# Performance work log

Measured on AMD Instinct MI355X. Metric: run time of the kernel, lower is better.

Reference implementation:

```python
import jax, jax.numpy as jnp
import numpy as np

B, S, D, H = 4, 1024, 1024, 16
HD = D // H
MAX_DIST, WIN, MAX_SPAN = 512, 256, 512
TEMP_SCALE = 0.01
EPS = 1e-5


def _ln(x, g, b):
    m = x.mean(-1, keepdims=True)
    v = ((x - m) ** 2).mean(-1, keepdims=True)
    return (x - m) * jax.lax.rsqrt(v + EPS) * g + b


def _heads(t):
    b, s, _ = t.shape
    return t.reshape(b, s, H, HD).transpose(0, 2, 1, 3)


def _merge(t):
    b, _, s, _ = t.shape
    return t.transpose(0, 2, 1, 3).reshape(b, s, D)


def _global_attn(x, Wq, bq, Wk, Wv, bv, Wo, bo):
    # MultiheadC with mask tensor passed -> is_causal=True SDPA (default 1/sqrt(HD) scale)
    q = _heads(x @ Wq.T + bq)
    k = _heads(x @ Wk.T)
    v = _heads(x @ Wv.T + bv)
    s = jnp.einsum('bhqd,bhkd->bhqk', q, k) / float(np.sqrt(HD))
    n = x.shape[1]
    causal = jnp.tril(jnp.ones((n, n), bool))
    s = jnp.where(causal, s, jnp.finfo(s.dtype).min)
    w = jax.nn.softmax(s, axis=-1)
    return _merge(jnp.einsum('bhqk,bhkd->bhqd', w, v)) @ Wo.T + bo


def _span_attn(q, k, v, temp):
    # AdaptiveSpan core: softmax(QK^T / temperature * head_dim**-0.25) V
    scale = HD ** -0.25
    qh, kh, vh = _heads(q), _heads(k), _heads(v)
    w = jax.nn.softmax(jnp.einsum('bhqd,bhkd->bhqk', qh, kh) / temp * scale, axis=-1)
    return _merge(jnp.einsum('bhqk,bhkd->bhqd', w, vh))


def _slide_win(local, span_mean, win, span_len, local_max):
    bx, sx, dx = local.shape
    temp = 1.0 + TEMP_SCALE * (1.0 - span_mean)  # sharpen=True branch
    outs = []
    for st in range(0, sx, win):  # static unrolled loop over windows (ragged slices)
        en = min(st + win, sx)
        wlen = en - st
        ks = max(0, st - span_len + win)
        ke = min(st + span_len, sx)
        klen = ke - ks
        eff = min(int(wlen * span_mean), wlen, klen, local_max)
        if eff <= 0:
            outs.append(jnp.zeros((bx, wlen, dx), local.dtype))
            continue
        o = _span_attn(local[:, st:st + eff], local[:, ks:ks + eff], local[:, ks:ks + eff], temp)
        if eff < wlen:
            o = jnp.concatenate([o, jnp.zeros((bx, wlen - eff, dx), local.dtype)], axis=1)
        outs.append(o)
    return jnp.concatenate(outs, axis=1)


def setup_inputs() -> dict:
    key = jax.random.key(0)
    ks = jax.random.split(key, 8)
    qkv_std = 1.0 / float(np.sqrt(HD))
    return {
        'x': jax.random.normal(ks[0], (B, S, D), jnp.float32),
        'ln_a_g': jnp.ones((D,), jnp.float32),
        'ln_a_b': jnp.zeros((D,), jnp.float32),
        'ln_b_g': jnp.ones((D,), jnp.float32),
        'ln_b_b': jnp.zeros((D,), jnp.float32),
        'Wq': jax.random.normal(ks[1], (D, D), jnp.float32) * qkv_std,
        'bq': jnp.zeros((D,), jnp.float32),
        'Wk': jax.random.normal(ks[2], (D, D), jnp.float32) * qkv_std,
        'Wv': jax.random.normal(ks[3], (D, D), jnp.float32) * qkv_std,
        'bv': jnp.zeros((D,), jnp.float32),
        'Wo': jax.random.normal(ks[4], (D, D), jnp.float32) * 0.02,
        'bo': jnp.zeros((D,), jnp.float32),
        'Wp': jax.random.normal(ks[5], (1, D), jnp.float32) * float(np.sqrt(2.0 / (D + 1))),
        'bp': jnp.zeros((1,), jnp.float32),
        'Wproj': jax.random.normal(ks[6], (D, 2 * D), jnp.float32) * 0.02,
        'bproj': jnp.zeros((D,), jnp.float32),
    }


def reference(x, ln_a_g, ln_a_b, ln_b_g, ln_b_b, Wq, bq, Wk, Wv, bv, Wo, bo, Wp, bp, Wproj, bproj):
    local = _ln(x, ln_a_g, ln_a_b)
    globe = _ln(x, ln_b_g, ln_b_b)
    globe_out = _global_attn(globe, Wq, bq, Wk, Wv, bv, Wo, bo)
    # Predictor: sigmoid(Linear(mean over seq))
    base_scale = jax.nn.sigmoid(globe_out.mean(axis=1) @ Wp.T + bp)  # [B, 1]
    span_scale = jnp.clip(base_scale, 0.0, 1.0)  # RL refine factor fixed at 1.0 (deterministic)
    span_mean = float(jnp.mean(span_scale))  # mirrors torch .item() host sync
    win = max(1, int(WIN * span_mean))
    span_len = max(1, int(MAX_SPAN * span_mean))
    local_max = min(MAX_DIST, span_len, win)
    local_out = _slide_win(local, span_mean, win, span_len, local_max)
    combined = jnp.concatenate([local_out, globe_out], axis=-1)
    return combined @ Wproj.T + bproj
```

## Files before the change

kernel.cpp:

```cpp
#include <hip/hip_runtime.h>
#include <math.h>

#define B_ 4
#define S_ 1024
#define D_ 1024
#define H_ 16
#define HD_ 64
#define BSD_ (B_*S_*D_)

using short8 = __attribute__((ext_vector_type(8))) short;
using f32x4  = __attribute__((ext_vector_type(4))) float;

#define MFMA16(a,b,c) __builtin_amdgcn_mfma_f32_16x16x32_bf16((a),(b),(c),0,0,0)

__device__ __forceinline__ ushort f2bf(float f) {
  uint u = __float_as_uint(f);
  return (ushort)((u + 0x7fffu + ((u >> 16) & 1u)) >> 16);
}
__device__ __forceinline__ float bf2f(ushort h) {
  return __uint_as_float(((uint)h) << 16);
}
__device__ __forceinline__ void split8(const float* p, short8* hi, short8* lo) {
  #pragma unroll
  for (int j = 0; j < 8; j++) {
    ushort h = f2bf(p[j]);
    (*hi)[j] = (short)h;
    (*lo)[j] = (short)f2bf(p[j] - bf2f(h));
  }
}
__device__ __forceinline__ void async_load16(const ushort* g, ushort* l) {
  __builtin_amdgcn_global_load_lds(
      (const __attribute__((address_space(1))) unsigned int*)g,
      (__attribute__((address_space(3))) unsigned int*)l, 16, 0, 0);
}

__device__ __forceinline__ float block_reduce_sum_256(float v, float* sbuf) {
  #pragma unroll
  for (int off = 32; off > 0; off >>= 1) v += __shfl_xor(v, off, 64);
  int lane = threadIdx.x & 63, wid = threadIdx.x >> 6;
  __syncthreads();
  if (lane == 0) sbuf[wid] = v;
  __syncthreads();
  return sbuf[0] + sbuf[1] + sbuf[2] + sbuf[3];
}

__device__ __forceinline__ void split4_store(const float4 a, ushort* orow, int c, int stride) {
  ushort4 hi, lo;
  hi.x = f2bf(a.x); hi.y = f2bf(a.y); hi.z = f2bf(a.z); hi.w = f2bf(a.w);
  lo.x = f2bf(a.x - bf2f(hi.x)); lo.y = f2bf(a.y - bf2f(hi.y));
  lo.z = f2bf(a.z - bf2f(hi.z)); lo.w = f2bf(a.w - bf2f(hi.w));
  *(ushort4*)(orow + c)          = hi;
  *(ushort4*)(orow + stride + c) = lo;
}

__global__ __launch_bounds__(256) void prep_kernel(
    const float* __restrict__ x,
    const float* __restrict__ ln_a_g, const float* __restrict__ ln_a_b,
    const float* __restrict__ ln_b_g, const float* __restrict__ ln_b_b,
    const float* __restrict__ Wq, const float* __restrict__ Wk,
    const float* __restrict__ Wv, const float* __restrict__ bq,
    const float* __restrict__ bv, const float* __restrict__ Wo,
    const float* __restrict__ Wproj,
    ushort* __restrict__ Acat, ushort* __restrict__ Bqkv,
    float* __restrict__ biascat, float* __restrict__ loc,
    ushort* __restrict__ B3, ushort* __restrict__ Bo) {
  __shared__ float sbuf[4];
  const int bx = blockIdx.x;
  const int t = threadIdx.x;
  if (bx < 4096) {
    const int row = bx;
    const int c = t*4;
    const float* xr = x + (size_t)row * D_;
    float4 v = *(const float4*)(xr + c);
    float s = v.x + v.y + v.z + v.w;
    const float mean = block_reduce_sum_256(s, sbuf) * (1.0f/D_);
    float4 dv = make_float4(v.x-mean, v.y-mean, v.z-mean, v.w-mean);
    float sq = dv.x*dv.x + dv.y*dv.y + dv.z*dv.z + dv.w*dv.w;
    const float var = block_reduce_sum_256(sq, sbuf) * (1.0f/D_);
    const float r = rsqrtf(var + 1e-5f);
    float4 gg = *(const float4*)(ln_b_g + c);
    float4 bb = *(const float4*)(ln_b_b + c);
    float4 n;
    n.x = dv.x*r*gg.x + bb.x; n.y = dv.y*r*gg.y + bb.y;
    n.z = dv.z*r*gg.z + bb.z; n.w = dv.w*r*gg.w + bb.w;
    split4_store(n, Acat + (size_t)row*2048, c, 1024);
  } else if (bx < 7168) {
    const int idx = (bx - 4096)*256 + t;
    const int n = idx >> 8;
    const int col4 = (idx & 255) << 2;
    const float* src = (n < 1024) ? (Wq + (size_t)n*1024)
                     : (n < 2048) ? (Wk + (size_t)(n-1024)*1024)
                                  : (Wv + (size_t)(n-2048)*1024);
    const float4 a = *(const float4*)(src + col4);
    split4_store(a, Bqkv + (size_t)n*2048, col4, 1024);
    if (idx < 3072)
      biascat[idx] = (idx < 1024) ? bq[idx] : (idx < 2048) ? 0.f : bv[idx-2048];
  } else if (bx < 11264) {
    const int row = bx - 7168;
    const float* xr = x + (size_t)row * D_;
    float v[4]; float s = 0.f;
    #pragma unroll
    for (int i = 0; i < 4; i++) { v[i] = xr[t + 256*i]; s += v[i]; }
    const float mean = block_reduce_sum_256(s, sbuf) * (1.0f/D_);
    float sq = 0.f;
    #pragma unroll
    for (int i = 0; i < 4; i++) { float d = v[i]-mean; sq += d*d; }
    const float var = block_reduce_sum_256(sq, sbuf) * (1.0f/D_);
    const float r = rsqrtf(var + 1e-5f);
    float* orow = loc + (size_t)row * D_;
    #pragma unroll
    for (int i = 0; i < 4; i++) {
      int c = t + 256*i;
      orow[c] = (v[i]-mean)*r*ln_a_g[c] + ln_a_b[c];
    }
  } else if (bx < 13312) {
    const int idx = (bx - 11264)*256 + t;
    const int row = idx >> 9;
    const int col4 = (idx & 511) << 2;
    const float4 a = *(const float4*)(Wproj + (size_t)row*2048 + col4);
    ushort4 hi;
    hi.x = f2bf(a.x); hi.y = f2bf(a.y); hi.z = f2bf(a.z); hi.w = f2bf(a.w);
    *(ushort4*)(B3 + (size_t)row*2048 + col4) = hi;
  } else {
    const int idx = (bx - 13312)*256 + t;
    const int n = idx >> 8;
    const int col4 = (idx & 255) << 2;
    const float4 a = *(const float4*)(Wo + (size_t)n*1024 + col4);
    split4_store(a, Bo + (size_t)n*2048, col4, 1024);
  }
}

#define BARRIER() asm volatile("s_barrier" ::: "memory")
#define VMW(n)  asm volatile("s_waitcnt vmcnt(" #n ")" ::: "memory")

#define STAGE4(k0, SBs) do { \
  _Pragma("unroll") \
  for (int i_ = 0; i_ < 2; ++i_) { \
    const int cid_ = wave*2 + i_, hl_ = cid_>>2, rs_ = cid_&3; \
    const int r0_ = (rs_>>1)*64 + (rs_&1)*16; \
    async_load16(A  + ((size_t)(bm + r0_ + lrow) << 11) + (hl_ << 10) + (k0) + sw, \
                 (SBs) + hl_*4096 + r0_*32); \
  } \
  _Pragma("unroll") \
  for (int i_ = 0; i_ < 2; ++i_) { \
    const int cid_ = wave*2 + i_, hl_ = cid_>>2, rs_ = cid_&3; \
    const int r0_ = (rs_>>1)*64 + (rs_&1)*16; \
    async_load16(Bw + ((size_t)(bn + r0_ + lrow) << 11) + (hl_ << 10) + (k0) + sw, \
                 (SBs) + 8192 + hl_*4096 + r0_*32); \
  } \
  _Pragma("unroll") \
  for (int i_ = 0; i_ < 2; ++i_) { \
    const int cid_ = wave*2 + i_, hl_ = cid_>>2, rs_ = cid_&3; \
    const int r1_ = (rs_>>1)*64 + (rs_&1)*16 + 32; \
    async_load16(Bw + ((size_t)(bn + r1_ + lrow) << 11) + (hl_ << 10) + (k0) + sw, \
                 (SBs) + 8192 + hl_*4096 + r1_*32); \
  } \
  _Pragma("unroll") \
  for (int i_ = 0; i_ < 2; ++i_) { \
    const int cid_ = wave*2 + i_, hl_ = cid_>>2, rs_ = cid_&3; \
    const int r1_ = (rs_>>1)*64 + (rs_&1)*16 + 32; \
    async_load16(A  + ((size_t)(bm + r1_ + lrow) << 11) + (hl_ << 10) + (k0) + sw, \
                 (SBs) + hl_*4096 + r1_*32); \
  } \
} while (0)

#define PH4(mh, nh, SBc, STG, WT) do { \
  short8 ah_[2], al_[2], bh_[2], bl_[2]; \
  _Pragma("unroll") \
  for (int m4_ = 0; m4_ < 2; ++m4_) { \
    const int ro_ = (wm*64 + (mh)*32 + m4_*16 + lm)*32 + rsw; \
    ah_[m4_] = *(const short8*)&(SBc)[ro_]; \
    al_[m4_] = *(const short8*)&(SBc)[4096 + ro_]; } \
  _Pragma("unroll") \
  for (int n2_ = 0; n2_ < 2; ++n2_) { \
    const int ro_ = (wn*64 + (nh)*32 + n2_*16 + lm)*32 + rsw; \
    bh_[n2_] = *(const short8*)&(SBc)[8192 + ro_]; \
    bl_[n2_] = *(const short8*)&(SBc)[12288 + ro_]; } \
  STG; \
  WT; \
  BARRIER(); \
  __builtin_amdgcn_s_setprio(1); \
  _Pragma("unroll") \
  for (int m4_ = 0; m4_ < 2; ++m4_) \
    _Pragma("unroll") \
    for (int n2_ = 0; n2_ < 2; ++n2_) { \
      f32x4 t_ = acc[(mh)*2+m4_][(nh)*2+n2_]; \
      t_ = MFMA16(ah_[m4_], bh_[n2_], t_); \
      t_ = MFMA16(al_[m4_], bh_[n2_], t_); \
      t_ = MFMA16(ah_[m4_], bl_[n2_], t_); \
      acc[(mh)*2+m4_][(nh)*2+n2_] = t_; } \
  __builtin_amdgcn_s_setprio(0); \
  BARRIER(); \
} while (0)

#define GROUP4(g, SBc, SBs) do { \
  const int k0n_ = (((g) + 1) & 31) * 32; \
  PH4(0, 0, (SBc), STAGE4(k0n_, (SBs)), VMW(10)); \
  PH4(0, 1, (SBc), ((void)0), VMW(8)); \
  PH4(1, 0, (SBc), ((void)0), ((void)0)); \
  PH4(1, 1, (SBc), ((void)0), VMW(4)); \
} while (0)

__global__ __launch_bounds__(256, 2) void qkv4_kernel(
    const ushort* __restrict__ A, const ushort* __restrict__ Bw,
    const float* __restrict__ bias,
    ushort* __restrict__ Qsp, ushort* __restrict__ Ksp,
    ushort* __restrict__ Vth, ushort* __restrict__ Vtl) {
  extern __shared__ __align__(16) ushort smem[];
  const int tid = threadIdx.x;
  const int bm = blockIdx.y * 128, bn = blockIdx.x * 128;
  const int wave = tid >> 6, lane = tid & 63;
  const int wm = wave >> 1, wn = wave & 1;
  const int lm = lane & 15, q = lane >> 4;
  const int lrow = lane >> 2;
  const int sw = (((lane & 3) ^ ((lane >> 3) & 3)) << 3);
  const int rsw = ((q ^ ((lm >> 1) & 3)) << 3);

  f32x4 acc[4][4];
  #pragma unroll
  for (int i = 0; i < 4; i++)
    #pragma unroll
    for (int j = 0; j < 4; j++)
      acc[i][j] = (f32x4){0.f,0.f,0.f,0.f};

  STAGE4(0, smem);
  VMW(4); BARRIER();

  #pragma unroll 1
  for (int g = 0; g < 32; g += 2) {
    GROUP4(g,     smem,         smem + 16384);
    GROUP4(g + 1, smem + 16384, smem);
  }
  VMW(0);
  __syncthreads();

  const int b = bm >> 10, s0 = bm & 1023;
  if (blockIdx.x < 16) {
    ushort* dst = (blockIdx.x < 8) ? Qsp : Ksp;
    #pragma unroll
    for (int mt = 0; mt < 4; mt++) {
      #pragma unroll
      for (int nt = 0; nt < 4; nt++) {
        const int n = bn + wn*64 + nt*16 + lm;
        const int h = (n >> 6) & 15;
        const int d = nt*16 + lm;
        const float bb = bias[n];
        #pragma unroll
        for (int reg = 0; reg < 4; reg++) {
          const int s = s0 + wm*64 + mt*16 + q*4 + reg;
          const float val = acc[mt][nt][reg] + bb;
          const ushort hi = f2bf(val);
          const ushort lo = f2bf(val - bf2f(hi));
          ushort* rp = dst + ((size_t)((b*16 + h)*1024 + s))*128;
          rp[d] = hi; rp[64 + d] = lo;
        }
      }
    }
  } else {
    ushort* Th = smem;
    ushort* Tl = smem + 8704;
    #pragma unroll
    for (int c = 0; c < 2; c++) {
      __syncthreads();
      if (wn == c) {
        #pragma unroll
        for (int mt = 0; mt < 4; mt++)
          #pragma unroll
          for (int nt = 0; nt < 4; nt++) {
            const int nl = nt*16 + lm;
            const float bb = bias[bn + c*64 + nl];
            #pragma unroll
            for (int reg = 0; reg < 4; reg++) {
              const int sl = wm*64 + mt*16 + q*4 + reg;
              const float val = acc[mt][nt][reg] + bb;
              const ushort hi = f2bf(val);
              const ushort lo = f2bf(val - bf2f(hi));
              Th[nl*136 + sl] = hi;
              Tl[nl*136 + sl] = lo;
            }
          }
      }
      __syncthreads();
      const int nl = tid >> 2, s32 = (tid & 3)*32;
      const int h = ((bn - 2048 + c*64) >> 6) & 15;
      const size_t drow = ((size_t)((b*16 + h)*64 + nl))*1024 + s0 + s32;
      #pragma unroll
      for (int j = 0; j < 4; j++) {
        *(short8*)(Vth + drow + j*8) = *(const short8*)&Th[nl*136 + s32 + j*8];
        *(short8*)(Vtl + drow + j*8) = *(const short8*)&Tl[nl*136 + s32 + j*8];
      }
    }
  }
}

__global__ __launch_bounds__(256) void mfma_gemm_qkv(
    const ushort* __restrict__ A, const ushort* __restrict__ Bw,
    const float* __restrict__ bias,
    ushort* __restrict__ Qsp, ushort* __restrict__ Ksp,
    ushort* __restrict__ Vth, ushort* __restrict__ Vtl, int Kh) {
  __shared__ __align__(16) ushort smem[17408];
  ushort* Ash = smem;
  ushort* Asl = smem + 4096;
  ushort* Bsh = smem + 8192;
  ushort* Bsl = smem + 12288;
  const int lda = 2*Kh;
  const int tid = threadIdx.x;
  const int bm = blockIdx.y * 128, bn = blockIdx.x * 128;
  const int wave = tid >> 6, lane = tid & 63;
  const int wm = wave >> 1, wn = wave & 1;
  const int lm = lane & 15, q = lane >> 4;
  const int lrow = lane >> 2;
  const int sw = (((lane & 3) ^ ((lane >> 3) & 3)) << 3);

  f32x4 acc[4][4];
  #pragma unroll
  for (int i = 0; i < 4; i++)
    #pragma unroll
    for (int j = 0; j < 4; j++)
      acc[i][j] = (f32x4){0.f,0.f,0.f,0.f};

  const ushort* Agh = A  + (size_t)(bm + wave*32 + lrow)*lda + sw;
  const ushort* Agl = Agh + Kh;
  const ushort* Bgh = Bw + (size_t)(bn + wave*32 + lrow)*lda + sw;
  const ushort* Bgl = Bgh + Kh;
  const size_t r16a = (size_t)16*lda;
  ushort* AhD0 = &Ash[(wave*32)*32];      ushort* AhD1 = &Ash[(wave*32+16)*32];
  ushort* AlD0 = &Asl[(wave*32)*32];      ushort* AlD1 = &Asl[(wave*32+16)*32];
  ushort* BhD0 = &Bsh[(wave*32)*32];      ushort* BhD1 = &Bsh[(wave*32+16)*32];
  ushort* BlD0 = &Bsl[(wave*32)*32];      ushort* BlD1 = &Bsl[(wave*32+16)*32];
  const int rsw  = ((q ^ ((lm >> 1) & 3)) << 3);
  const int aoff = (wm*64 + lm)*32 + rsw;
  const int boff = (wn*64 + lm)*32 + rsw;

  for (int k0 = 0; k0 < Kh; k0 += 32) {
    __syncthreads();
    async_load16(Agh + k0, AhD0);
    async_load16(Agh + r16a + k0, AhD1);
    async_load16(Agl + k0, AlD0);
    async_load16(Agl + r16a + k0, AlD1);
    async_load16(Bgh + k0, BhD0);
    async_load16(Bgh + r16a + k0, BhD1);
    async_load16(Bgl + k0, BlD0);
    async_load16(Bgl + r16a + k0, BlD1);
    __syncthreads();
    short8 ah[4], al[4], bh[4], bl[4];
    #pragma unroll
    for (int mt = 0; mt < 4; mt++) {
      ah[mt] = *(const short8*)&Ash[aoff + mt*512];
      al[mt] = *(const short8*)&Asl[aoff + mt*512];
    }
    #pragma unroll
    for (int nt = 0; nt < 4; nt++) {
      bh[nt] = *(const short8*)&Bsh[boff + nt*512];
      bl[nt] = *(const short8*)&Bsl[boff + nt*512];
    }
    #pragma unroll
    for (int mt = 0; mt < 4; mt++)
      #pragma unroll
      for (int nt = 0; nt < 4; nt++) {
        f32x4 a = acc[mt][nt];
        a = MFMA16(ah[mt], bh[nt], a);
        a = MFMA16(al[mt], bh[nt], a);
        a = MFMA16(ah[mt], bl[nt], a);
        acc[mt][nt] = a;
      }
  }

  const int b = bm >> 10, s0 = bm & 1023;
  if (blockIdx.x < 16) {
    ushort* dst = (blockIdx.x < 8) ? Qsp : Ksp;
    #pragma unroll
    for (int mt = 0; mt < 4; mt++) {
      #pragma unroll
      for (int nt = 0; nt < 4; nt++) {
        const int n = bn + wn*64 + nt*16 + lm;
        const int h = (n >> 6) & 15;
        const int d = nt*16 + lm;
        const float bb = bias[n];
        #pragma unroll
        for (int reg = 0; reg < 4; reg++) {
          const int s = s0 + wm*64 + mt*16 + q*4 + reg;
          const float val = acc[mt][nt][reg] + bb;
          const ushort hi = f2bf(val);
          const ushort lo = f2bf(val - bf2f(hi));
          ushort* rp = dst + ((size_t)((b*16 + h)*1024 + s))*128;
          rp[d] = hi; rp[64 + d] = lo;
        }
      }
    }
  } else {
    ushort* Th = smem;
    ushort* Tl = smem + 8704;
    #pragma unroll
    for (int c = 0; c < 2; c++) {
      __syncthreads();
      if (wn == c) {
        #pragma unroll
        for (int mt = 0; mt < 4; mt++)
          #pragma unroll
          for (int nt = 0; nt < 4; nt++) {
            const int nl = nt*16 + lm;
            const float bb = bias[bn + c*64 + nl];
            #pragma unroll
            for (int reg = 0; reg < 4; reg++) {
              const int sl = wm*64 + mt*16 + q*4 + reg;
              const float val = acc[mt][nt][reg] + bb;
              const ushort hi = f2bf(val);
              const ushort lo = f2bf(val - bf2f(hi));
              Th[nl*136 + sl] = hi;
              Tl[nl*136 + sl] = lo;
            }
          }
      }
      __syncthreads();
      const int nl = tid >> 2, s32 = (tid & 3)*32;
      const int h = ((bn - 2048 + c*64) >> 6) & 15;
      const size_t drow = ((size_t)((b*16 + h)*64 + nl))*1024 + s0 + s32;
      #pragma unroll
      for (int j = 0; j < 4; j++) {
        *(short8*)(Vth + drow + j*8) = *(const short8*)&Th[nl*136 + s32 + j*8];
        *(short8*)(Vtl + drow + j*8) = *(const short8*)&Tl[nl*136 + s32 + j*8];
      }
    }
  }
}

__global__ __launch_bounds__(256) void mfma_gemm2(
    const ushort* __restrict__ A, const ushort* __restrict__ Bw,
    const float* __restrict__ bias, float* __restrict__ C,
    int Kh, int ldc, ushort* __restrict__ aux) {
  __shared__ __align__(16) ushort Ash[64*32];
  __shared__ __align__(16) ushort Asl[64*32];
  __shared__ __align__(16) ushort Bsh[128*32];
  __shared__ __align__(16) ushort Bsl[128*32];
  const int lda = 2*Kh;
  const int tid = threadIdx.x;
  const int bm = blockIdx.y * 64, bn = blockIdx.x * 128;
  const int wave = tid >> 6, lane = tid & 63;
  const int lm = lane & 15, q = lane >> 4;
  const int lrow = lane >> 2;
  const int sw = (((lane & 3) ^ ((lane >> 3) & 3)) << 3);

  f32x4 acc[4][2];
  #pragma unroll
  for (int i = 0; i < 4; i++)
    #pragma unroll
    for (int j = 0; j < 2; j++)
      acc[i][j] = (f32x4){0.f,0.f,0.f,0.f};

  const ushort* gsrc[6];
  ushort* ldst[6];
  #pragma unroll
  for (int i = 0; i < 6; i++) {
    const int s = wave*6 + i;
    const ushort* gp; ushort* lp;
    if (s < 4)       { gp = A  + (size_t)(bm + s*16 + lrow)*lda + sw;           lp = &Ash[(s*16)*32]; }
    else if (s < 8)  { gp = A  + (size_t)(bm + (s-4)*16 + lrow)*lda + Kh + sw;  lp = &Asl[((s-4)*16)*32]; }
    else if (s < 16) { gp = Bw + (size_t)(bn + (s-8)*16 + lrow)*lda + sw;       lp = &Bsh[((s-8)*16)*32]; }
    else             { gp = Bw + (size_t)(bn + (s-16)*16 + lrow)*lda + Kh + sw; lp = &Bsl[((s-16)*16)*32]; }
    gsrc[i] = gp; ldst[i] = lp;
  }
  const int rsw = ((q ^ ((lm >> 1) & 3)) << 3);
  const int aoff = lm*32 + rsw;
  const int boff = (wave*32 + lm)*32 + rsw;

  for (int k0 = 0; k0 < Kh; k0 += 32) {
    __syncthreads();
    #pragma unroll
    for (int i = 0; i < 6; i++) async_load16(gsrc[i] + k0, ldst[i]);
    __syncthreads();
    short8 ah[4], al[4], bh[2], bl[2];
    #pragma unroll
    for (int mt = 0; mt < 4; mt++) {
      ah[mt] = *(const short8*)&Ash[aoff + mt*512];
      al[mt] = *(const short8*)&Asl[aoff + mt*512];
    }
    #pragma unroll
    for (int nt = 0; nt < 2; nt++) {
      bh[nt] = *(const short8*)&Bsh[boff + nt*512];
      bl[nt] = *(const short8*)&Bsl[boff + nt*512];
    }
    #pragma unroll
    for (int mt = 0; mt < 4; mt++)
      #pragma unroll
      for (int nt = 0; nt < 2; nt++) {
        f32x4 a = acc[mt][nt];
        a = MFMA16(ah[mt], bh[nt], a);
        a = MFMA16(al[mt], bh[nt], a);
        a = MFMA16(ah[mt], bl[nt], a);
        acc[mt][nt] = a;
      }
  }

  #pragma unroll
  for (int mt = 0; mt < 4; mt++) {
    #pragma unroll
    for (int nt = 0; nt < 2; nt++) {
      const int n = bn + wave*32 + nt*16 + lm;
      const float bb = bias ? bias[n] : 0.f;
      #pragma unroll
      for (int reg = 0; reg < 4; reg++) {
        const int m = bm + mt*16 + q*4 + reg;
        const float val = acc[mt][nt][reg] + bb;
        C[(size_t)m*ldc + n] = val;
        if (aux) aux[(size_t)m*2048 + 1024 + n] = f2bf(val);
      }
    }
  }
}

__global__ __launch_bounds__(256) void mfma_gemm(
    const ushort* __restrict__ A, const ushort* __restrict__ Bw,
    const float* __restrict__ bias, float* __restrict__ C,
    int K, int ldc) {
  __shared__ __align__(16) ushort As[64*32];
  __shared__ __align__(16) ushort Bs[128*32];
  const int tid = threadIdx.x;
  const int bm = blockIdx.y * 64, bn = blockIdx.x * 128;
  const int wave = tid >> 6, lane = tid & 63;
  const int lm = lane & 15, q = lane >> 4;
  const int lrow = lane >> 2;
  const int sw = (((lane & 3) ^ ((lane >> 3) & 3)) << 3);

  f32x4 acc[4][2];
  #pragma unroll
  for (int i = 0; i < 4; i++)
    #pragma unroll
    for (int j = 0; j < 2; j++)
      acc[i][j] = (f32x4){0.f,0.f,0.f,0.f};

  const ushort* gsrc[3];
  ushort* ldst[3];
  #pragma unroll
  for (int i = 0; i < 3; i++) {
    const int s = wave*3 + i;
    const ushort* gp; ushort* lp;
    if (s < 4) { gp = A  + (size_t)(bm + s*16 + lrow)*K + sw;     lp = &As[(s*16)*32]; }
    else       { gp = Bw + (size_t)(bn + (s-4)*16 + lrow)*K + sw; lp = &Bs[((s-4)*16)*32]; }
    gsrc[i] = gp; ldst[i] = lp;
  }
  const int rsw = ((q ^ ((lm >> 1) & 3)) << 3);
  const int aoff = lm*32 + rsw;
  const int boff = (wave*32 + lm)*32 + rsw;

  for (int k0 = 0; k0 < K; k0 += 32) {
    __syncthreads();
    #pragma unroll
    for (int i = 0; i < 3; i++) async_load16(gsrc[i] + k0, ldst[i]);
    __syncthreads();
    short8 af[4], bf[2];
    #pragma unroll
    for (int mt = 0; mt < 4; mt++) af[mt] = *(const short8*)&As[aoff + mt*512];
    #pragma unroll
    for (int nt = 0; nt < 2; nt++) bf[nt] = *(const short8*)&Bs[boff + nt*512];
    #pragma unroll
    for (int mt = 0; mt < 4; mt++)
      #pragma unroll
      for (int nt = 0; nt < 2; nt++)
        acc[mt][nt] = MFMA16(af[mt], bf[nt], acc[mt][nt]);
  }

  #pragma unroll
  for (int mt = 0; mt < 4; mt++) {
    #pragma unroll
    for (int nt = 0; nt < 2; nt++) {
      const int n = bn + wave*32 + nt*16 + lm;
      const float bb = bias ? bias[n] : 0.f;
      #pragma unroll
      for (int reg = 0; reg < 4; reg++) {
        const int m = bm + mt*16 + q*4 + reg;
        C[(size_t)m*ldc + n] = acc[mt][nt][reg] + bb;
      }
    }
  }
}

__device__ __forceinline__ void attn_unit(
    int qt, int kt, int w, int lm, int q,
    const short8 qh[2], const short8 ql[2],
    const ushort* Kc, const ushort* Vc, float* Pf,
    f32x4 of[4], float mst[4], float lst[4]) {
  f32x4 sS[4];
  #pragma unroll
  for (int nt = 0; nt < 4; nt++) {
    const ushort* kr = &Kc[(nt*16 + lm)*136 + q*8];
    const short8 kh0 = *(const short8*)(kr);
    const short8 kh1 = *(const short8*)(kr + 32);
    const short8 kl0 = *(const short8*)(kr + 64);
    const short8 kl1 = *(const short8*)(kr + 96);
    f32x4 a = (f32x4){0.f,0.f,0.f,0.f};
    a = MFMA16(qh[0], kh0, a);
    a = MFMA16(ql[0], kh0, a);
    a = MFMA16(qh[0], kl0, a);
    a = MFMA16(qh[1], kh1, a);
    a = MFMA16(ql[1], kh1, a);
    a = MFMA16(qh[1], kl1, a);
    sS[nt] = a;
  }
  const int ktbase = kt*64;
  const int qrow0 = qt*64 + w*16 + q*4;
  #pragma unroll
  for (int rm = 0; rm < 4; rm++) {
    const int qrow = qrow0 + rm;
    float v[4];
    #pragma unroll
    for (int nt = 0; nt < 4; nt++) {
      const int kcol = ktbase + nt*16 + lm;
      const float x = sS[nt][rm]*0.125f;
      v[nt] = (kcol <= qrow) ? x : -INFINITY;
    }
    float tm = fmaxf(fmaxf(v[0],v[1]), fmaxf(v[2],v[3]));
    #pragma unroll
    for (int off = 1; off < 16; off <<= 1) tm = fmaxf(tm, __shfl_xor(tm, off, 64));
    const float nm = fmaxf(mst[rm], tm);
    const float alpha = __expf(mst[rm] - nm);
    float ps = 0.f;
    #pragma unroll
    for (int nt = 0; nt < 4; nt++) {
      float p = __expf(v[nt] - nm);
      sS[nt][rm] = p;
      ps += p;
    }
    #pragma unroll
    for (int off = 1; off < 16; off <<= 1) ps += __shfl_xor(ps, off, 64);
    lst[rm] = lst[rm]*alpha + ps;
    mst[rm] = nm;
    #pragma unroll
    for (int nt = 0; nt < 4; nt++) of[nt][rm] *= alpha;
  }
  #pragma unroll
  for (int rm = 0; rm < 4; rm++)
    #pragma unroll
    for (int nt = 0; nt < 4; nt++)
      Pf[(w*16 + q*4 + rm)*66 + nt*16 + lm] = sS[nt][rm];
  short8 ph[2], pl[2];
  {
    const float* prow = &Pf[(w*16 + lm)*66];
    float pv[16];
    *(float4*)&pv[0]  = *(const float4*)(prow + q*8);
    *(float4*)&pv[4]  = *(const float4*)(prow + q*8 + 4);
    *(float4*)&pv[8]  = *(const float4*)(prow + 32 + q*8);
    *(float4*)&pv[12] = *(const float4*)(prow + 32 + q*8 + 4);
    split8(&pv[0], &ph[0], &pl[0]);
    split8(&pv[8], &ph[1], &pl[1]);
  }
  #pragma unroll
  for (int nt = 0; nt < 4; nt++) {
    const ushort* vr = &Vc[(nt*16 + lm)*136 + q*8];
    const short8 vh0 = *(const short8*)(vr);
    const short8 vh1 = *(const short8*)(vr + 32);
    const short8 vl0 = *(const short8*)(vr + 64);
    const short8 vl1 = *(const short8*)(vr + 96);
    f32x4 a = of[nt];
    a = MFMA16(ph[0], vh0, a);
    a = MFMA16(pl[0], vh0, a);
    a = MFMA16(ph[0], vl0, a);
    a = MFMA16(ph[1], vh1, a);
    a = MFMA16(pl[1], vh1, a);
    a = MFMA16(ph[1], vl1, a);
    of[nt] = a;
  }
}

__global__ __launch_bounds__(256) void gattn_mfma(
    const ushort* __restrict__ Qsp, const ushort* __restrict__ Ksp,
    const ushort* __restrict__ Vth, const ushort* __restrict__ Vtl,
    ushort* __restrict__ Aout) {
  __shared__ __align__(16) ushort Kc[64*136];
  __shared__ __align__(16) ushort Vc[64*136];
  __shared__ __align__(16) float  Pf[64*66];
  const int bh = blockIdx.y;
  const int b = bh >> 4, h = bh & 15;
  const int tid = threadIdx.x;
  const int w = tid >> 6, lane = tid & 63;
  const int lm = lane & 15, q = lane >> 4;
  const ushort* Qb_ = Qsp + (size_t)bh * (1024*128);
  const ushort* Kb_ = Ksp + (size_t)bh * (1024*128);
  const ushort* Vhb = Vth + (size_t)bh * (64*1024);
  const ushort* Vlb = Vtl + (size_t)bh * (64*1024);
  const int qtA = 15 - blockIdx.x;
  const int qtB = blockIdx.x;

  short8 qhA[2], qlA[2], qhB[2], qlB[2];
  {
    const ushort* qr = Qb_ + (size_t)(qtA*64 + w*16 + lm)*128 + q*8;
    qhA[0] = *(const short8*)(qr);
    qhA[1] = *(const short8*)(qr + 32);
    qlA[0] = *(const short8*)(qr + 64);
    qlA[1] = *(const short8*)(qr + 96);
    const ushort* qr2 = Qb_ + (size_t)(qtB*64 + w*16 + lm)*128 + q*8;
    qhB[0] = *(const short8*)(qr2);
    qhB[1] = *(const short8*)(qr2 + 32);
    qlB[0] = *(const short8*)(qr2 + 64);
    qlB[1] = *(const short8*)(qr2 + 96);
  }
  f32x4 ofA[4], ofB[4];
  float mstA[4], lstA[4], mstB[4], lstB[4];
  #pragma unroll
  for (int nt = 0; nt < 4; nt++) {
    ofA[nt] = (f32x4){0.f,0.f,0.f,0.f};
    ofB[nt] = (f32x4){0.f,0.f,0.f,0.f};
  }
  #pragma unroll
  for (int rm = 0; rm < 4; rm++) {
    mstA[rm] = -INFINITY; lstA[rm] = 0.f;
    mstB[rm] = -INFINITY; lstB[rm] = 0.f;
  }

  for (int kt = 0; kt <= qtA; ++kt) {
    __syncthreads();
    #pragma unroll
    for (int i = 0; i < 4; i++) {
      const int slot = i*256 + tid;
      const int row = slot >> 4, c8 = slot & 15;
      *(float4*)&Kc[row*136 + c8*8] =
          *(const float4*)(Kb_ + (size_t)(kt*64 + row)*128 + c8*8);
      const ushort* vsrc = ((c8 < 8) ? Vhb : Vlb) + (size_t)row*1024 + kt*64 + (c8&7)*8;
      *(float4*)&Vc[row*136 + c8*8] = *(const float4*)vsrc;
    }
    __syncthreads();
    attn_unit(qtA, kt, w, lm, q, qhA, qlA, Kc, Vc, Pf, ofA, mstA, lstA);
    if (kt <= qtB)
      attn_unit(qtB, kt, w, lm, q, qhB, qlB, Kc, Vc, Pf, ofB, mstB, lstB);
  }

  #pragma unroll
  for (int rm = 0; rm < 4; rm++) {
    const float invA = 1.0f / lstA[rm];
    const int sA = qtA*64 + w*16 + q*4 + rm;
    ushort* arow = Aout + ((size_t)(b*1024 + sA))*2048 + h*64;
    #pragma unroll
    for (int nt = 0; nt < 4; nt++) {
      const float val = ofA[nt][rm] * invA;
      const ushort hi = f2bf(val);
      arow[nt*16 + lm] = hi;
      arow[1024 + nt*16 + lm] = f2bf(val - bf2f(hi));
    }
    const float invB = 1.0f / lstB[rm];
    const int sB = qtB*64 + w*16 + q*4 + rm;
    ushort* brow = Aout + ((size_t)(b*1024 + sB))*2048 + h*64;
    #pragma unroll
    for (int nt = 0; nt < 4; nt++) {
      const float val = ofB[nt][rm] * invB;
      const ushort hi = f2bf(val);
      brow[nt*16 + lm] = hi;
      brow[1024 + nt*16 + lm] = f2bf(val - bf2f(hi));
    }
  }
}

__global__ __launch_bounds__(256) void seqmean1_kernel(const float* __restrict__ g,
                                                       float* __restrict__ part) {
  const int d = blockIdx.x*256 + threadIdx.x;
  const int sc = blockIdx.y;
  const int b = blockIdx.z;
  const float* p = g + ((size_t)b*S_ + sc*128)*D_ + d;
  float s = 0.f;
  #pragma unroll 4
  for (int i = 0; i < 128; i++) s += p[(size_t)i*D_];
  part[((size_t)(b*8 + sc))*D_ + d] = s;
}
__global__ __launch_bounds__(256) void seqmean2_kernel(const float* __restrict__ part,
                                                       float* __restrict__ mbd) {
  const int d = blockIdx.x*256 + threadIdx.x;
  const int b = blockIdx.y;
  float s = 0.f;
  #pragma unroll
  for (int i = 0; i < 8; i++) s += part[((size_t)(b*8 + i))*D_ + d];
  mbd[b*D_ + d] = s * (1.0f/S_);
}

__global__ __launch_bounds__(256) void predictor_kernel(
    const float* __restrict__ mbd, const float* __restrict__ Wp,
    const float* __restrict__ bp, float* __restrict__ fpar, int* __restrict__ ipar) {
  __shared__ float sbuf[4];
  __shared__ float sdots[4];
  const int tid = threadIdx.x;
  for (int b = 0; b < 4; b++) {
    float psum = 0.f;
    for (int d = tid; d < D_; d += 256) psum += mbd[b*D_ + d]*Wp[d];
    float tot = block_reduce_sum_256(psum, sbuf);
    if (tid == 0) sdots[b] = tot;
  }
  __syncthreads();
  if (tid == 0) {
    float smv = 0.f;
    for (int b = 0; b < 4; b++) {
      float z = sdots[b] + bp[0];
      smv += 1.0f/(1.0f + expf(-z));
    }
    smv *= 0.25f;
    int win = max(1, (int)(256.0f*smv));
    int span_len = max(1, (int)(512.0f*smv));
    int local_max = min(512, min(span_len, win));
    float temp = 1.0f + 0.01f*(1.0f - smv);
    int n_win = (S_ + win - 1)/win;
    fpar[0] = smv; fpar[1] = temp;
    ipar[0] = win; ipar[1] = span_len; ipar[2] = local_max; ipar[3] = n_win;
  }
}

#define LDP 68
__global__ __launch_bounds__(256) void lattn_kernel(
    const float* __restrict__ Lc, ushort* __restrict__ Out,
    const int* __restrict__ ip, const float* __restrict__ fpp) {
  __shared__ __align__(16) float Qs[HD_][LDP];
  __shared__ __align__(16) float KPs[64][LDP];
  __shared__ __align__(16) float Vs[64][LDP];
  const int n_win = ip[3];
  const int win = ip[0], span_len = ip[1], local_max = ip[2];
  const float sm = fpp[0], temp = fpp[1];
  const int bh = blockIdx.y;
  const int b = bh >> 4, h = bh & 15;
  const int tid = threadIdx.x;
  const int tx = tid & 15, ty = tid >> 4;
  const float sc = 0.35355339059327373f / temp;
  for (int w = blockIdx.x; w < n_win; w += gridDim.x) {
    const int st = w * win;
    const int en = min(st + win, S_); const int wlen = en - st;
    const int ks = max(0, st - span_len + win);
    const int ke = min(st + span_len, S_); const int klen = ke - ks;
    int eff = (int)((double)wlen * (double)sm);
    eff = min(min(eff, wlen), min(klen, local_max));
    if (eff > 0) {
      const int nt = (eff + 63) >> 6;
      for (int qt = 0; qt < nt; ++qt) {
        const int qn = min(64, eff - qt*64);
        __syncthreads();
        #pragma unroll
        for (int c = 0; c < 4; c++) {
          int f = tid + c*256;
          int r = f >> 4;
          int dc = (f & 15) << 2;
          float4 q4 = make_float4(0.f,0.f,0.f,0.f);
          if (r < qn) q4 = *(const float4*)(Lc + ((size_t)(b*S_ + st + qt*64 + r)) * D_ + h*HD_ + dc);
          Qs[dc+0][r]=q4.x; Qs[dc+1][r]=q4.y; Qs[dc+2][r]=q4.z; Qs[dc+3][r]=q4.w;
        }
        float o[4][4] = {{0.f,0.f,0.f,0.f},{0.f,0.f,0.f,0.f},{0.f,0.f,0.f,0.f},{0.f,0.f,0.f,0.f}};
        float mrow[4], lrow[4];
        #pragma unroll
        for (int i=0;i<4;i++){ mrow[i] = -INFINITY; lrow[i] = 0.f; }
        for (int kt = 0; kt < nt; ++kt) {
          const int kn = min(64, eff - kt*64);
          __syncthreads();
          #pragma unroll
          for (int c = 0; c < 4; c++) {
            int f = tid + c*256;
            int r = f >> 4;
            int dc = (f & 15) << 2;
            float4 k4 = make_float4(0.f,0.f,0.f,0.f);
            if (r < kn) k4 = *(const float4*)(Lc + ((size_t)(b*S_ + ks + kt*64 + r)) * D_ + h*HD_ + dc);
            KPs[dc+0][r]=k4.x; KPs[dc+1][r]=k4.y; KPs[dc+2][r]=k4.z; KPs[dc+3][r]=k4.w;
            *(float4*)&Vs[r][dc] = k4;
          }
          __syncthreads();
          float s[4][4] = {{0.f,0.f,0.f,0.f},{0.f,0.f,0.f,0.f},{0.f,0.f,0.f,0.f},{0.f,0.f,0.f,0.f}};
          #pragma unroll 8
          for (int d = 0; d < HD_; ++d) {
            const float4 a  = *(const float4*)&Qs[d][ty*4];
            const float4 bb = *(const float4*)&KPs[d][tx*4];
            const float av[4]={a.x,a.y,a.z,a.w};
            const float bv[4]={bb.x,bb.y,bb.z,bb.w};
            #pragma unroll
            for (int i=0;i<4;i++)
              #pragma unroll
              for (int j=0;j<4;j++)
                s[i][j] += av[i]*bv[j];
          }
          #pragma unroll
          for (int i=0;i<4;i++) {
            #pragma unroll
            for (int j=0;j<4;j++) {
              float lg = s[i][j]*sc;
              if (kt*64 + tx*4 + j >= eff) lg = -INFINITY;
              s[i][j] = lg;
            }
          }
          #pragma unroll
          for (int i=0;i<4;i++) {
            float tm = fmaxf(fmaxf(s[i][0],s[i][1]), fmaxf(s[i][2],s[i][3]));
            #pragma unroll
            for (int off=1; off<16; off<<=1) tm = fmaxf(tm, __shfl_xor(tm, off, 64));
            const float nm = fmaxf(mrow[i], tm);
            const float alpha = __expf(mrow[i]-nm);
            float ps = 0.f;
            #pragma unroll
            for (int j=0;j<4;j++){ float p = __expf(s[i][j]-nm); s[i][j]=p; ps += p; }
            #pragma unroll
            for (int off=1; off<16; off<<=1) ps += __shfl_xor(ps, off, 64);
            lrow[i] = lrow[i]*alpha + ps;
            mrow[i] = nm;
            #pragma unroll
            for (int j=0;j<4;j++) o[i][j] *= alpha;
          }
          __syncthreads();
          #pragma unroll
          for (int i=0;i<4;i++)
            #pragma unroll
            for (int j=0;j<4;j++)
              KPs[tx*4+j][ty*4+i] = s[i][j];
          __syncthreads();
          #pragma unroll 8
          for (int kk = 0; kk < 64; ++kk) {
            const float4 a  = *(const float4*)&KPs[kk][ty*4];
            const float4 bb = *(const float4*)&Vs[kk][tx*4];
            const float av[4]={a.x,a.y,a.z,a.w};
            const float bv[4]={bb.x,bb.y,bb.z,bb.w};
            #pragma unroll
            for (int i=0;i<4;i++)
              #pragma unroll
              for (int j=0;j<4;j++)
                o[i][j] += av[i]*bv[j];
          }
        }
        #pragma unroll
        for (int i=0;i<4;i++){
          const int r = ty*4 + i;
          if (r < qn) {
            const float inv = 1.0f / lrow[i];
            ushort4 ov;
            ov.x = f2bf(o[i][0]*inv); ov.y = f2bf(o[i][1]*inv);
            ov.z = f2bf(o[i][2]*inv); ov.w = f2bf(o[i][3]*inv);
            *(ushort4*)(Out + ((size_t)(b*S_ + st + qt*64 + r)) * 2048 + h*HD_ + tx*4) = ov;
          }
        }
      }
    }
    const ushort4 z = {0,0,0,0};
    for (int r = max(eff, 0) + ty; r < wlen; r += 16)
      *(ushort4*)(Out + ((size_t)(b*S_ + st + r)) * 2048 + h*HD_ + tx*4) = z;
  }
}

extern "C" void kernel_launch(void* const* d_in, const int* in_sizes, int n_in,
                              void* d_out, int out_size, void* d_ws, size_t ws_size,
                              hipStream_t stream) {
  const float* x      = (const float*)d_in[0];
  const float* ln_a_g = (const float*)d_in[1];
  const float* ln_a_b = (const float*)d_in[2];
  const float* ln_b_g = (const float*)d_in[3];
  const float* ln_b_b = (const float*)d_in[4];
  const float* Wq     = (const float*)d_in[5];
  const float* bq     = (const float*)d_in[6];
  const float* Wk     = (const float*)d_in[7];
  const float* Wv     = (const float*)d_in[8];
  const float* bv     = (const float*)d_in[9];
  const float* Wo     = (const float*)d_in[10];
  const float* bo     = (const float*)d_in[11];
  const float* Wp     = (const float*)d_in[12];
  const float* bp     = (const float*)d_in[13];
  const float* Wproj  = (const float*)d_in[14];
  const float* bproj  = (const float*)d_in[15];
  float* out = (float*)d_out;
  float* ws  = (float*)d_ws;
  ushort* wsu = (ushort*)d_ws;

  ushort* Qsp = wsu;
  ushort* Ksp = wsu + 8388608;
  ushort* Vth = wsu + 16777216;
  ushort* Vtl = wsu + 20971520;
  ushort* B3  = (ushort*)(ws + 12582912);
  float* glo  = ws + 16777216;
  float* loc  = ws + 20971520;
  float* biascat = ws + 25165824;
  float* mbd  = biascat + 4096;
  float* fpar = mbd + 4096;
  int*   ipar = (int*)(fpar + 8);
  ushort* Acat  = (ushort*)(ws + 25182208);
  ushort* Bqkv  = Acat + 12582912;
  ushort* Bo    = Bqkv + 9437184;
  float*  part = (float*)Acat;
  ushort* A3  = wsu;

  const dim3 blk(256);

  static int qkv_path = -1;
  if (qkv_path < 0) {
    hipError_t e = hipFuncSetAttribute(
        reinterpret_cast<const void*>(qkv4_kernel),
        hipFuncAttributeMaxDynamicSharedMemorySize, 65536);
    qkv_path = (e == hipSuccess) ? 1 : 0;
  }

  prep_kernel<<<dim3(14336), blk, 0, stream>>>(
      x, ln_a_g, ln_a_b, ln_b_g, ln_b_b, Wq, Wk, Wv, bq, bv, Wo, Wproj,
      Acat, Bqkv, biascat, loc, B3, Bo);
  if (qkv_path)
    qkv4_kernel<<<dim3(24, 32), blk, 65536, stream>>>(
        Acat, Bqkv, biascat, Qsp, Ksp, Vth, Vtl);
  else
    mfma_gemm_qkv<<<dim3(24, 32), blk, 0, stream>>>(Acat, Bqkv, biascat,
                                                    Qsp, Ksp, Vth, Vtl, 1024);
  gattn_mfma<<<dim3(8, 64), blk, 0, stream>>>(Qsp, Ksp, Vth, Vtl, Acat);
  mfma_gemm2<<<dim3(8, 64), blk, 0, stream>>>(Acat, Bo, bo, glo, 1024, 1024, A3);
  seqmean1_kernel<<<dim3(4, 8, B_), blk, 0, stream>>>(glo, part);
  seqmean2_kernel<<<dim3(4, B_), blk, 0, stream>>>(part, mbd);
  predictor_kernel<<<dim3(1), blk, 0, stream>>>(mbd, Wp, bp, fpar, ipar);
  lattn_kernel<<<dim3(64, B_*H_), blk, 0, stream>>>(loc, A3, ipar, fpar);
  mfma_gemm<<<dim3(8, 64), blk, 0, stream>>>(A3, B3, bproj, out, 2048, 1024);
}
```

Measured before the change: 441.5 us.

## Replace paired-tile global attention with one query tile per block

Adds a causal attention kernel in which each block handles a single 64-row query tile and loops over the key tiles up to the diagonal, launched on a 16x64 grid instead of 8x64. The old kernel appears to pair query tiles per block to balance causal work. The new layout doubles the block count to raise occupancy and parallelism across CUs. In exchange, work per block is imbalanced, since late tiles do up to 16 key iterations and early ones do one, and K/V tiles are reloaded per block without sharing across paired tiles.

```diff
diff --git a/kernel.cpp b/kernel.cpp
--- a/kernel.cpp
+++ b/kernel.cpp
@@ -659,6 +659,69 @@
     a = MFMA16(pl[1], vh1, a);
     a = MFMA16(ph[1], vl1, a);
     of[nt] = a;
+  }
+}
+
+__global__ __launch_bounds__(256) void gattn1q(
+    const ushort* __restrict__ Qsp, const ushort* __restrict__ Ksp,
+    const ushort* __restrict__ Vth, const ushort* __restrict__ Vtl,
+    ushort* __restrict__ Aout) {
+  __shared__ __align__(16) ushort Kc[64*136];
+  __shared__ __align__(16) ushort Vc[64*136];
+  __shared__ __align__(16) float  Pf[64*66];
+  const int bh = blockIdx.y;
+  const int b = bh >> 4, h = bh & 15;
+  const int qt = blockIdx.x;
+  const int tid = threadIdx.x;
+  const int w = tid >> 6, lane = tid & 63;
+  const int lm = lane & 15, q = lane >> 4;
+  const ushort* Qb_ = Qsp + (size_t)bh * (1024*128);
+  const ushort* Kb_ = Ksp + (size_t)bh * (1024*128);
+  const ushort* Vhb = Vth + (size_t)bh * (64*1024);
+  const ushort* Vlb = Vtl + (size_t)bh * (64*1024);
+
+  short8 qh[2], ql[2];
+  {
+    const ushort* qr = Qb_ + (size_t)(qt*64 + w*16 + lm)*128 + q*8;
+    qh[0] = *(const short8*)(qr);
+    qh[1] = *(const short8*)(qr + 32);
+    ql[0] = *(const short8*)(qr + 64);
+    ql[1] = *(const short8*)(qr + 96);
+  }
+  f32x4 of[4];
+  float mst[4], lst[4];
+  #pragma unroll
+  for (int nt = 0; nt < 4; nt++) of[nt] = (f32x4){0.f,0.f,0.f,0.f};
+  #pragma unroll
+  for (int rm = 0; rm < 4; rm++) { mst[rm] = -INFINITY; lst[rm] = 0.f; }
+
+  for (int kt = 0; kt <= qt; ++kt) {
+    __syncthreads();
+    #pragma unroll
+    for (int i = 0; i < 4; i++) {
+      const int slot = i*256 + tid;
+      const int row = slot >> 4, c8 = slot & 15;
+      *(float4*)&Kc[row*136 + c8*8] =
+          *(const float4*)(Kb_ + (size_t)(kt*64 + row)*128 + c8*8);
+      const ushort* vsrc = ((c8 < 8) ? Vhb : Vlb) + (size_t)row*1024 + kt*64 + (c8&7)*8;
+      *(float4*)&Vc[row*136 + c8*8] = *(const float4*)vsrc;
+    }
+    __syncthreads();
+    attn_unit(qt, kt, w, lm, q, qh, ql, Kc, Vc, Pf, of, mst, lst);
+  }
+
+  #pragma unroll
+  for (int rm = 0; rm < 4; rm++) {
+    const float inv = 1.0f / lst[rm];
+    const int s = qt*64 + w*16 + q*4 + rm;
+    ushort* arow = Aout + ((size_t)(b*1024 + s))*2048 + h*64;
+    #pragma unroll
+    for (int nt = 0; nt < 4; nt++) {
+      const float val = of[nt][rm] * inv;
+      const ushort hi = f2bf(val);
+      arow[nt*16 + lm] = hi;
+      arow[1024 + nt*16 + lm] = f2bf(val - bf2f(hi));
+    }
   }
 }
 
@@ -991,7 +1054,7 @@
   else
     mfma_gemm_qkv<<<dim3(24, 32), blk, 0, stream>>>(Acat, Bqkv, biascat,
                                                     Qsp, Ksp, Vth, Vtl, 1024);
-  gattn_mfma<<<dim3(8, 64), blk, 0, stream>>>(Qsp, Ksp, Vth, Vtl, Acat);
+  gattn1q<<<dim3(16, 64), blk, 0, stream>>>(Qsp, Ksp, Vth, Vtl, Acat);
   mfma_gemm2<<<dim3(8, 64), blk, 0, stream>>>(Acat, Bo, bo, glo, 1024, 1024, A3);
   seqmean1_kernel<<<dim3(4, 8, B_), blk, 0, stream>>>(glo, part);
   seqmean2_kernel<<<dim3(4, B_), blk, 0, stream>>>(part, mbd);
```

Result: slower. 501.5 us (+13.6%).
